# Optimization experiments

Measured on AMD Instinct MI355X. Metric: run time of the kernel, lower is better.

## Reference

```python
import jax, jax.numpy as jnp
import numpy as np

B, C, H, W = 16, 64, 128, 128


def setup_inputs() -> dict:
    key = jax.random.key(0)
    k1, k2, k3 = jax.random.split(key, 3)
    return {
        "template_map": jax.random.normal(k1, (B, C, H, W), dtype=jnp.float32),
        "roi_map": jax.random.normal(k2, (B, C, H, W), dtype=jnp.float32),
        "gamma": jnp.zeros((1,), dtype=jnp.float32),
        "omega": jnp.zeros((1,), dtype=jnp.float32),
        "conv_w": jax.random.normal(k3, (C, 2 * C), dtype=jnp.float32) * 0.05,
        "conv_b": jnp.zeros((C,), dtype=jnp.float32),
    }


def _chan_attn(x):
    # x: [B, C, H, W] -> attention over channels [B, C, C] and flat values [B, C, N]
    b, c, h, w = x.shape
    v = x.reshape(b, c, h * w)
    energy = jnp.einsum('bcn,bdn->bcd', v, v)  # [B, C, C]
    energy_new = jnp.max(energy, axis=-1, keepdims=True) - energy
    attn = jax.nn.softmax(energy_new, axis=-1)
    return attn, v


def reference(template_map, roi_map, gamma, omega, conv_w, conv_b):
    b, c, th, tw = template_map.shape
    _, _, rh, rw = roi_map.shape
    t_attn, t_v = _chan_attn(template_map)
    r_attn, r_v = _chan_attn(roi_map)
    # cross application: roi attention reweights template channels, and vice versa
    t_out = jnp.einsum('bcd,bdn->bcn', r_attn, t_v).reshape(b, c, th, tw)
    t_out = gamma * t_out + template_map
    r_out = jnp.einsum('bcd,bdn->bcn', t_attn, r_v).reshape(b, c, rh, rw)
    r_out = omega * r_out + roi_map
    fused = jnp.concatenate([t_out, r_out], axis=1)  # [B, 2C, H, W]
    # 1x1 conv == channel-mixing einsum
    out = jnp.einsum('bchw,oc->bohw', fused, conv_w) + conv_b[None, :, None, None]
    return out
```

## Files before the change

kernel.cpp:

```cpp
#include <hip/hip_runtime.h>

typedef __attribute__((ext_vector_type(8))) short short8;
typedef __attribute__((ext_vector_type(4))) float floatx4;
typedef unsigned int uint;
typedef unsigned short ushort;

#define BATCH 16
#define CH 64
#define NPIX 16384
#define TWOC 128

__device__ __forceinline__ ushort f2bf(float f) {
    uint u = __float_as_uint(f);
    u += 0x7FFFu + ((u >> 16) & 1u);
    return (ushort)(u >> 16);
}

__global__ __launch_bounds__(256) void gram_kernel(
    const float* __restrict__ tmap, const float* __restrict__ rmap,
    const float* __restrict__ gamma, const float* __restrict__ omega,
    float* __restrict__ G)
{
    const int map = blockIdx.y;
    const float mult = (map == 0) ? omega[0] : gamma[0];
    if (mult == 0.f) return;

    __shared__ float tile[64][68];
    const int chunk = blockIdx.x;
    const int b     = blockIdx.z;
    const float* x = (map == 0 ? tmap : rmap) + (size_t)b * CH * NPIX + chunk * 512;
    const int t  = threadIdx.x;
    const int ti = t >> 4;
    const int tj = t & 15;

    float acc[4][4];
#pragma unroll
    for (int i = 0; i < 4; ++i)
#pragma unroll
        for (int j = 0; j < 4; ++j) acc[i][j] = 0.f;

    for (int tt = 0; tt < 8; ++tt) {
        const int col0 = tt * 64;
#pragma unroll
        for (int k = 0; k < 16; ++k) {
            int e = t + 256 * k;
            int c = e >> 6, col = e & 63;
            tile[c][col] = x[(size_t)c * NPIX + col0 + col];
        }
        __syncthreads();
#pragma unroll 8
        for (int n = 0; n < 64; n += 2) {
            float2 av[4], bv[4];
#pragma unroll
            for (int i = 0; i < 4; ++i) av[i] = *(const float2*)&tile[ti + 16 * i][n];
#pragma unroll
            for (int j = 0; j < 4; ++j) bv[j] = *(const float2*)&tile[tj + 16 * j][n];
#pragma unroll
            for (int i = 0; i < 4; ++i)
#pragma unroll
                for (int j = 0; j < 4; ++j) {
                    acc[i][j] += av[i].x * bv[j].x;
                    acc[i][j] += av[i].y * bv[j].y;
                }
        }
        __syncthreads();
    }
    float* Gp = G + ((size_t)(b * 2 + map) << 12);
#pragma unroll
    for (int i = 0; i < 4; ++i)
#pragma unroll
        for (int j = 0; j < 4; ++j)
            atomicAdd(&Gp[(ti + 16 * i) * 64 + (tj + 16 * j)], acc[i][j]);
}

__global__ __launch_bounds__(128) void finalize_kernel(
    const float* __restrict__ G, const float* __restrict__ gamma,
    const float* __restrict__ omega, const float* __restrict__ conv_w,
    ushort* __restrict__ Mtf)
{
    __shared__ float attn[2][64][64];
    const int b = blockIdx.x;
    const int t = threadIdx.x;
    const float gam = gamma[0], om = omega[0];
    {
        const int map = t >> 6, i = t & 63;
        const float need = (map == 0) ? om : gam;
        if (need != 0.f) {
            const float* Grow = G + ((size_t)(b * 2 + map) << 12) + i * 64;
            float mn = Grow[0];
            for (int j = 1; j < 64; ++j) mn = fminf(mn, Grow[j]);
            float s = 0.f;
            for (int j = 0; j < 64; ++j) s += expf(mn - Grow[j]);
            const float inv = 1.f / s;
            for (int j = 0; j < 64; ++j) attn[map][i][j] = expf(mn - Grow[j]) * inv;
        }
    }
    __syncthreads();
    for (int idx = t; idx < 8192; idx += 128) {
        const int e     = idx & 7;
        const int l     = (idx >> 3) & 63;
        const int mi    = (idx >> 9) & 3;
        const int kstep = idx >> 11;
        const int row = mi * 16 + (l & 15);
        const int k   = kstep * 32 + (l >> 4) * 8 + e;
        const float* wrow = conv_w + row * TWOC;
        float v = wrow[k];
        if (k < 64) {
            if (gam != 0.f) {
                float dot = 0.f;
                for (int c = 0; c < 64; ++c) dot += wrow[c] * attn[1][c][k];
                v += gam * dot;
            }
        } else {
            const int d = k - 64;
            if (om != 0.f) {
                float dot = 0.f;
                for (int c = 0; c < 64; ++c) dot += wrow[64 + c] * attn[0][c][d];
                v += om * dot;
            }
        }
        Mtf[(size_t)b * 8192 + idx] = f2bf(v);
    }
}

__global__ __launch_bounds__(256, 3) void out_kernel(
    const float* __restrict__ tmap, const float* __restrict__ rmap,
    const ushort* __restrict__ Mtf, const float* __restrict__ conv_b,
    float* __restrict__ out)
{
    __shared__ __align__(16) ushort Ms[8192];
    __shared__ __align__(16) ushort Xs[8 * 256 * 8];

    const int b   = blockIdx.y;
    const int t   = threadIdx.x;
    const int px0 = blockIdx.x * 256;

    {
        const uint4* src = (const uint4*)(Mtf + (size_t)b * 8192);
        uint4* dst = (uint4*)Ms;
#pragma unroll
        for (int i = 0; i < 4; ++i) dst[t + 256 * i] = src[t + 256 * i];
    }

    const int w  = t >> 6;
    const int l  = t & 63;
    const int lg = l >> 4;
    const int lj = l & 15;

    const float* xsrc0 = tmap + (size_t)b * CH * NPIX + px0 + t;
    const float* xsrc1 = rmap + (size_t)b * CH * NPIX + px0 + t;

    floatx4 acc[4][4];
#pragma unroll
    for (int mi = 0; mi < 4; ++mi)
#pragma unroll
        for (int nj = 0; nj < 4; ++nj) acc[mi][nj] = (floatx4){0.f, 0.f, 0.f, 0.f};

    float bias[4][4];
#pragma unroll
    for (int mi = 0; mi < 4; ++mi)
#pragma unroll
        for (int r = 0; r < 4; ++r) bias[mi][r] = conv_b[mi * 16 + lg * 4 + r];

#pragma unroll
    for (int h = 0; h < 2; ++h) {
        const float* s = (h == 0) ? xsrc0 : xsrc1;
#pragma unroll
        for (int i = 0; i < 8; ++i) {
            float v[8];
#pragma unroll
            for (int e = 0; e < 8; ++e) v[e] = s[(size_t)(i * 8 + e) * NPIX];
            short8 pk;
#pragma unroll
            for (int e = 0; e < 8; ++e) pk[e] = (short)f2bf(v[e]);
            *(short8*)&Xs[(i * 256 + t) * 8] = pk;
        }
        __syncthreads();

#pragma unroll
        for (int ks = 0; ks < 2; ++ks) {
            short8 a[4];
#pragma unroll
            for (int mi = 0; mi < 4; ++mi)
                a[mi] = *(const short8*)&Ms[(((h * 2 + ks) * 4 + mi) * 64 + l) * 8];
#pragma unroll
            for (int nj = 0; nj < 4; ++nj) {
                const short8 bb = *(const short8*)
                    &Xs[((ks * 4 + lg) * 256 + w * 64 + nj * 16 + lj) * 8];
#pragma unroll
                for (int mi = 0; mi < 4; ++mi)
                    acc[mi][nj] = __builtin_amdgcn_mfma_f32_16x16x32_bf16(
                        a[mi], bb, acc[mi][nj], 0, 0, 0);
            }
        }
        __syncthreads();
    }

#pragma unroll
    for (int mi = 0; mi < 4; ++mi)
#pragma unroll
        for (int nj = 0; nj < 4; ++nj) {
            const int px = px0 + w * 64 + nj * 16 + lj;
#pragma unroll
            for (int r = 0; r < 4; ++r) {
                const int och = mi * 16 + lg * 4 + r;
                out[((size_t)b * CH + och) * NPIX + px] = acc[mi][nj][r] + bias[mi][r];
            }
        }
}

extern "C" void kernel_launch(void* const* d_in, const int* in_sizes, int n_in,
                              void* d_out, int out_size, void* d_ws, size_t ws_size,
                              hipStream_t stream) {
    const float* tmap   = (const float*)d_in[0];
    const float* rmap   = (const float*)d_in[1];
    const float* gamma  = (const float*)d_in[2];
    const float* omega  = (const float*)d_in[3];
    const float* conv_w = (const float*)d_in[4];
    const float* conv_b = (const float*)d_in[5];
    float* out = (float*)d_out;

    float*  G   = (float*)d_ws;
    ushort* Mtf = (ushort*)((char*)d_ws + (size_t)BATCH * 2 * 4096 * sizeof(float));

    hipMemsetAsync(d_ws, 0, (size_t)BATCH * 2 * 4096 * sizeof(float), stream);

    gram_kernel<<<dim3(32, 2, BATCH), 256, 0, stream>>>(tmap, rmap, gamma, omega, G);
    finalize_kernel<<<dim3(BATCH), 128, 0, stream>>>(G, gamma, omega, conv_w, Mtf);
    out_kernel<<<dim3(64, BATCH), 256, 0, stream>>>(tmap, rmap, Mtf, conv_b, out);
}
```

Before: 55.40 us.

## Drop LDS staging in out_kernel; load inputs and weights straight into MFMA registers

The output kernel no longer stages the bf16 weight matrix and the converted input tiles in shared memory. Each lane loads its MFMA operands directly from global memory (weights from Mtf, activations from the maps with bf16 conversion in registers), which removes both __syncthreads barriers and the LDS traffic. Global loads are now 16-lane row segments of 64 bytes instead of full 256-thread coalesced rows, and the weights are reread per block from cache rather than shared. Without LDS, more blocks per CU may fit.

```diff
diff --git a/kernel.cpp b/kernel.cpp
--- a/kernel.cpp
+++ b/kernel.cpp
@@ -128,27 +128,15 @@
     const ushort* __restrict__ Mtf, const float* __restrict__ conv_b,
     float* __restrict__ out)
 {
-    __shared__ __align__(16) ushort Ms[8192];
-    __shared__ __align__(16) ushort Xs[8 * 256 * 8];
-
     const int b   = blockIdx.y;
     const int t   = threadIdx.x;
-    const int px0 = blockIdx.x * 256;
-
-    {
-        const uint4* src = (const uint4*)(Mtf + (size_t)b * 8192);
-        uint4* dst = (uint4*)Ms;
-#pragma unroll
-        for (int i = 0; i < 4; ++i) dst[t + 256 * i] = src[t + 256 * i];
-    }
-
-    const int w  = t >> 6;
-    const int l  = t & 63;
-    const int lg = l >> 4;
-    const int lj = l & 15;
-
-    const float* xsrc0 = tmap + (size_t)b * CH * NPIX + px0 + t;
-    const float* xsrc1 = rmap + (size_t)b * CH * NPIX + px0 + t;
+    const int w   = t >> 6;
+    const int l   = t & 63;
+    const int lg  = l >> 4;
+    const int lj  = l & 15;
+    const int pxw = blockIdx.x * 256 + w * 64;
+
+    const ushort* mbase = Mtf + (size_t)b * 8192;
 
     floatx4 acc[4][4];
 #pragma unroll
@@ -156,57 +144,46 @@
 #pragma unroll
         for (int nj = 0; nj < 4; ++nj) acc[mi][nj] = (floatx4){0.f, 0.f, 0.f, 0.f};
 
-    float bias[4][4];
-#pragma unroll
-    for (int mi = 0; mi < 4; ++mi)
-#pragma unroll
-        for (int r = 0; r < 4; ++r) bias[mi][r] = conv_b[mi * 16 + lg * 4 + r];
-
 #pragma unroll
     for (int h = 0; h < 2; ++h) {
-        const float* s = (h == 0) ? xsrc0 : xsrc1;
-#pragma unroll
-        for (int i = 0; i < 8; ++i) {
-            float v[8];
-#pragma unroll
-            for (int e = 0; e < 8; ++e) v[e] = s[(size_t)(i * 8 + e) * NPIX];
-            short8 pk;
-#pragma unroll
-            for (int e = 0; e < 8; ++e) pk[e] = (short)f2bf(v[e]);
-            *(short8*)&Xs[(i * 256 + t) * 8] = pk;
-        }
-        __syncthreads();
-
+        const float* src = ((h == 0) ? tmap : rmap) + (size_t)b * CH * NPIX;
 #pragma unroll
         for (int ks = 0; ks < 2; ++ks) {
             short8 a[4];
 #pragma unroll
             for (int mi = 0; mi < 4; ++mi)
-                a[mi] = *(const short8*)&Ms[(((h * 2 + ks) * 4 + mi) * 64 + l) * 8];
+                a[mi] = *(const short8*)&mbase[((((h * 2 + ks) * 4 + mi) * 64) + l) * 8];
+
 #pragma unroll
             for (int nj = 0; nj < 4; ++nj) {
-                const short8 bb = *(const short8*)
-                    &Xs[((ks * 4 + lg) * 256 + w * 64 + nj * 16 + lj) * 8];
+                const float* cbase = src + (size_t)(ks * 32 + lg * 8) * NPIX
+                                         + pxw + nj * 16 + lj;
+                float v[8];
+#pragma unroll
+                for (int e = 0; e < 8; ++e) v[e] = cbase[(size_t)e * NPIX];
+                short8 bb;
+#pragma unroll
+                for (int e = 0; e < 8; ++e) bb[e] = (short)f2bf(v[e]);
 #pragma unroll
                 for (int mi = 0; mi < 4; ++mi)
                     acc[mi][nj] = __builtin_amdgcn_mfma_f32_16x16x32_bf16(
                         a[mi], bb, acc[mi][nj], 0, 0, 0);
             }
         }
-        __syncthreads();
-    }
-
-#pragma unroll
-    for (int mi = 0; mi < 4; ++mi)
-#pragma unroll
-        for (int nj = 0; nj < 4; ++nj) {
-            const int px = px0 + w * 64 + nj * 16 + lj;
-#pragma unroll
-            for (int r = 0; r < 4; ++r) {
-                const int och = mi * 16 + lg * 4 + r;
-                out[((size_t)b * CH + och) * NPIX + px] = acc[mi][nj][r] + bias[mi][r];
-            }
-        }
+    }
+
+#pragma unroll
+    for (int mi = 0; mi < 4; ++mi) {
+#pragma unroll
+        for (int r = 0; r < 4; ++r) {
+            const int och = mi * 16 + lg * 4 + r;
+            const float bv = conv_b[och];
+            float* orow = out + ((size_t)b * CH + och) * NPIX;
+#pragma unroll
+            for (int nj = 0; nj < 4; ++nj)
+                orow[pxw + nj * 16 + lj] = acc[mi][nj][r] + bv;
+        }
+    }
 }
 
 extern "C" void kernel_launch(void* const* d_in, const int* in_sizes, int n_in,
```

Measured after the change: 53.52 us. -3.4%, faster.
